# Optimization experiments

Hardware: AMD Instinct MI355X
Metric: run time of the kernel (lower is better)

Reference implementation:

```python
import jax, jax.numpy as jnp
import numpy as np

SEQ, D, H, P, FINAL = 2048, 1024, 16, 64, 1024


def setup_inputs() -> dict:
    key = jax.random.key(0)
    k_x, k_q, k_k, k_v, k_w = jax.random.split(key, 5)
    return {
        "x": jax.random.normal(k_x, (SEQ, D), dtype=jnp.float32),
        "Qw": jax.random.uniform(k_q, (H, D, P), dtype=jnp.float32),
        "Kw": jax.random.uniform(k_k, (H, D, P), dtype=jnp.float32),
        "Vw": jax.random.uniform(k_v, (H, D, P), dtype=jnp.float32),
        "W_fin": jax.random.normal(k_w, (H * P, FINAL), dtype=jnp.float32) * (1.0 / np.sqrt(H * P)),
        "b_fin": jnp.zeros((FINAL,), dtype=jnp.float32),
    }


def reference(x, Qw, Kw, Vw, W_fin, b_fin):
    # x: [S, D]; Qw/Kw/Vw: [H, D, P]
    Q = jnp.einsum("sd,hdp->hsp", x, Qw)  # [H, S, P]
    K = jnp.einsum("sd,hdp->hsp", x, Kw)
    V = jnp.einsum("sd,hdp->hsp", x, Vw)
    p_dim = K.shape[-1]
    # sigmoid attention: no row-wise normalization, scale by P (not sqrt(P))
    score = jax.nn.sigmoid(jnp.einsum("hsp,htp->hst", Q, K) / p_dim)  # [H, S, S]
    attn = jnp.einsum("hst,htp->hsp", score, V)  # [H, S, P]
    # faithful raw reshape (torch .reshape(seq, -1) on contiguous [H, S, P])
    concat = attn.reshape(x.shape[0], -1)  # [S, H*P]
    return concat @ W_fin + b_fin  # [S, FINAL]
```

## Files before the change

### kernel.cpp

```cpp
#include <hip/hip_runtime.h>
#include <hip/hip_bf16.h>

#define SEQL 2048
#define DMODEL 1024
#define NH 16
#define HEADP 64
#define FINALD 1024

using bf16x8 = __attribute__((ext_vector_type(8))) short;
using f32x4  = __attribute__((ext_vector_type(4))) float;
using s16x4  = __attribute__((ext_vector_type(4))) short;

#define WAITV(N) asm volatile("s_waitcnt vmcnt(" #N ")" ::: "memory")

__device__ __forceinline__ f32x4 mfma16(bf16x8 a, bf16x8 b, f32x4 c) {
  return __builtin_amdgcn_mfma_f32_16x16x32_bf16(a, b, c, 0, 0, 0);
}

__device__ __forceinline__ unsigned short f2bf(float f) {
  return __builtin_bit_cast(unsigned short, __float2bfloat16(f));
}

__device__ __forceinline__ void gload16(const void* g, void* l) {
  __builtin_amdgcn_global_load_lds(
      (const __attribute__((address_space(1))) void*)g,
      (__attribute__((address_space(3))) void*)l, 16, 0, 0);
}

__global__ __launch_bounds__(256) void k_prep(
    const float* __restrict__ Qw, const float* __restrict__ Kw,
    const float* __restrict__ Vw, const float* __restrict__ Wf,
    const float* __restrict__ x,
    unsigned short* __restrict__ Wt, unsigned short* __restrict__ WfT,
    unsigned short* __restrict__ xb) {
  __shared__ float tile[64][65];
  int z = blockIdx.z;
  int t = threadIdx.x;
  if (z == 4) {
    long i0 = ((long)blockIdx.y * 16 + blockIdx.x) * 2048 + t;
#pragma unroll
    for (int k = 0; k < 8; ++k) {
      long i = i0 + k * 256;
      float4 v = reinterpret_cast<const float4*>(x)[i];
      ushort4 o;
      o.x = f2bf(v.x); o.y = f2bf(v.y); o.z = f2bf(v.z); o.w = f2bf(v.w);
      reinterpret_cast<ushort4*>(xb)[i] = o;
    }
    return;
  }
  const float* src; unsigned short* dst;
  int C, tr = blockIdx.x * 64, tc;
  if (z < 3) {
    const float* s3 = (z == 0) ? Qw : (z == 1) ? Kw : Vw;
    src = s3 + (long)blockIdx.y * 65536;
    dst = Wt + (long)z * 1048576 + (long)blockIdx.y * 65536;
    C = 64; tc = 0;
  } else {
    src = Wf; dst = WfT; C = 1024; tc = blockIdx.y * 64;
  }
  const int R = 1024;
  int r0 = t >> 4, c4 = (t & 15) * 4;
#pragma unroll
  for (int i = 0; i < 4; ++i) {
    int r = i * 16 + r0;
    float4 v = *reinterpret_cast<const float4*>(src + (long)(tr + r) * C + tc + c4);
    tile[r][c4 + 0] = v.x; tile[r][c4 + 1] = v.y;
    tile[r][c4 + 2] = v.z; tile[r][c4 + 3] = v.w;
  }
  __syncthreads();
  int r4 = (t & 15) * 4, cc0 = t >> 4;
#pragma unroll
  for (int i = 0; i < 4; ++i) {
    int c = i * 16 + cc0;
    ushort4 o;
    o.x = f2bf(tile[r4 + 0][c]); o.y = f2bf(tile[r4 + 1][c]);
    o.z = f2bf(tile[r4 + 2][c]); o.w = f2bf(tile[r4 + 3][c]);
    *reinterpret_cast<ushort4*>(dst + (long)(tc + c) * R + tr + r4) = o;
  }
}

template <int EPI>
__global__ __launch_bounds__(256) void k_gemm(
    const unsigned short* __restrict__ A,
    const unsigned short* __restrict__ Bt,
    int K,
    unsigned short* __restrict__ Qb,
    unsigned short* __restrict__ Kb,
    unsigned short* __restrict__ Vtb,
    const float* __restrict__ bias,
    float* __restrict__ outf) {
  __shared__ char lds[49152];
  int flat = blockIdx.y * 16 + blockIdx.x;
  int cpx = (gridDim.x * gridDim.y) >> 3;
  flat = (flat & 7) * cpx + (flat >> 3);
  int m0 = (flat & 15) << 7, n0 = (flat >> 4) * 64;
  int t = threadIdx.x;
  int l = t & 63, w = t >> 6;
  int r = l & 15, g = l >> 4;
  int wr = w >> 1, wc = w & 1;

  const unsigned short* Arow = A + (long)m0 * K;
  const unsigned short* Brow = Bt + (long)n0 * K;
  int rr = l >> 2;
  int c8s = (((l & 3) ^ ((l >> 3) & 3)) * 8);

  auto stage = [&](int buf, int k0) {
    char* base = lds + buf * 24576;
#pragma unroll
    for (int kk = 0; kk < 2; ++kk) {
      char* dA = base + kk * 8192 + w * 2048;
      char* dB = base + 16384 + kk * 4096 + w * 1024;
      int kc = k0 + kk * 32 + c8s;
      gload16(Arow + (long)(w * 32 + rr) * K + kc, dA);
      gload16(Arow + (long)(w * 32 + 16 + rr) * K + kc, dA + 1024);
      gload16(Brow + (long)(w * 16 + rr) * K + kc, dB);
    }
  };

  int xk = (r >> 1) & 3;
  f32x4 acc[4][2] = {};
  int cur = 0, NK = K / 64;
  stage(0, 0);
  for (int kt = 0; kt < NK; ++kt) {
    __builtin_amdgcn_s_barrier();
    if (kt + 1 < NK) {
      stage(cur ^ 1, (kt + 1) * 64);
      WAITV(6);
    } else {
      WAITV(0);
    }
    __builtin_amdgcn_s_barrier();
    __builtin_amdgcn_sched_barrier(0);
    const char* base = lds + cur * 24576;
#pragma unroll
    for (int kk = 0; kk < 2; ++kk) {
      const char* As = base + kk * 8192;
      const char* Bs = base + 16384 + kk * 4096;
      bf16x8 af[4], bb[2];
#pragma unroll
      for (int i = 0; i < 4; ++i)
        af[i] = *reinterpret_cast<const bf16x8*>(As + (wr * 64 + i * 16 + r) * 64 + ((g ^ xk) * 16));
#pragma unroll
      for (int i = 0; i < 2; ++i)
        bb[i] = *reinterpret_cast<const bf16x8*>(Bs + (wc * 32 + i * 16 + r) * 64 + ((g ^ xk) * 16));
#pragma unroll
      for (int mi = 0; mi < 4; ++mi)
#pragma unroll
        for (int ni = 0; ni < 2; ++ni)
          acc[mi][ni] = mfma16(af[mi], bb[ni], acc[mi][ni]);
    }
    cur ^= 1;
  }

  if constexpr (EPI == 0) {
    int which = n0 >> 10;
    int hb = (n0 & 1023) >> 6;
    if (which < 2) {
      unsigned short* dst = (which == 0 ? Qb : Kb) + (long)hb * SEQL * HEADP;
#pragma unroll
      for (int mi = 0; mi < 4; ++mi) {
        int s0 = m0 + wr * 64 + mi * 16 + g * 4;
#pragma unroll
        for (int ni = 0; ni < 2; ++ni) {
          int p = wc * 32 + ni * 16 + r;
#pragma unroll
          for (int v = 0; v < 4; ++v)
            dst[(long)(s0 + v) * HEADP + p] = f2bf(acc[mi][ni][v]);
        }
      }
    } else {
      unsigned short* dst = Vtb + (long)hb * HEADP * SEQL;
#pragma unroll
      for (int mi = 0; mi < 4; ++mi) {
        int s0 = m0 + wr * 64 + mi * 16 + g * 4;
#pragma unroll
        for (int ni = 0; ni < 2; ++ni) {
          int p = wc * 32 + ni * 16 + r;
          ushort4 pk;
          pk.x = f2bf(acc[mi][ni][0]); pk.y = f2bf(acc[mi][ni][1]);
          pk.z = f2bf(acc[mi][ni][2]); pk.w = f2bf(acc[mi][ni][3]);
          *reinterpret_cast<ushort4*>(dst + (long)p * SEQL + s0) = pk;
        }
      }
    }
  } else {
#pragma unroll
    for (int ni = 0; ni < 2; ++ni) {
      int c = n0 + wc * 32 + ni * 16 + r;
      float bv = bias[c];
#pragma unroll
      for (int mi = 0; mi < 4; ++mi) {
        int s0 = m0 + wr * 64 + mi * 16 + g * 4;
#pragma unroll
        for (int v = 0; v < 4; ++v)
          outf[(long)(s0 + v) * FINALD + c] = acc[mi][ni][v] + bv;
      }
    }
  }
}

__global__ __launch_bounds__(256) void k_attn(
    const unsigned short* __restrict__ Qb,
    const unsigned short* __restrict__ Kb,
    const unsigned short* __restrict__ Vtb,
    unsigned short* __restrict__ Ab) {
  __shared__ char lds[40960];
  int b = blockIdx.x;
  int xcd = b & 7, j = b >> 3;
  int h = (xcd << 1) | (j & 1);
  int sblk = j >> 1;
  int lane = threadIdx.x & 63, wave = threadIdx.x >> 6;
  int r = lane & 15, g = lane >> 4;
  int q0 = sblk * 64 + wave * 16;
  const unsigned short* Qh = Qb + ((long)h * SEQL + q0) * HEADP;
  const unsigned short* Kh = Kb + (long)h * SEQL * HEADP;
  const unsigned short* Vh = Vtb + (long)h * HEADP * SEQL;

  bf16x8 qf0 = *reinterpret_cast<const bf16x8*>(Qh + (long)r * HEADP + g * 8);
  bf16x8 qf1 = *reinterpret_cast<const bf16x8*>(Qh + (long)r * HEADP + 32 + g * 8);

  f32x4 z4 = {0.f, 0.f, 0.f, 0.f};
  f32x4 oacc[4] = {z4, z4, z4, z4};
  char* slab = lds + 32768 + wave * 2048;
  int swz = (r & 7) << 4;
  const float CLN = -0.02254211001389005f;

  int sub = lane >> 3, chunk = lane & 7;
  auto stage = [&](int buf, int t0) {
    char* kb = lds + buf * 16384 + wave * 2048;
    char* vb = kb + 8192;
#pragma unroll
    for (int jj = 0; jj < 2; ++jj) {
      int row = wave * 16 + jj * 8 + sub;
      int sw = (chunk ^ (row & 7)) * 8;
      gload16(Kh + (long)(t0 + row) * HEADP + sw, kb + jj * 1024);
      gload16(Vh + (long)row * SEQL + t0 + sw, vb + jj * 1024);
    }
  };

  int cur = 0;
  stage(0, 0);
  for (int t0 = 0; t0 < SEQL; t0 += 64) {
    __builtin_amdgcn_s_barrier();
    if (t0 + 64 < SEQL) {
      stage(cur ^ 1, t0 + 64);
      WAITV(4);
    } else {
      WAITV(0);
    }
    __builtin_amdgcn_s_barrier();
    __builtin_amdgcn_sched_barrier(0);

    const char* kb = lds + cur * 16384;
    const char* vb = kb + 8192;
    f32x4 s[4] = {z4, z4, z4, z4};
    __builtin_amdgcn_s_setprio(1);
#pragma unroll
    for (int tb = 0; tb < 4; ++tb) {
      const char* krow = kb + (tb * 16 + r) * 128;
      bf16x8 k0 = *reinterpret_cast<const bf16x8*>(krow + ((g ^ (r & 7)) * 16));
      bf16x8 k1 = *reinterpret_cast<const bf16x8*>(krow + (((4 + g) ^ (r & 7)) * 16));
      s[tb] = mfma16(k0, qf0, s[tb]);
      s[tb] = mfma16(k1, qf1, s[tb]);
    }
    __builtin_amdgcn_s_setprio(0);
#pragma unroll
    for (int tb = 0; tb < 4; ++tb) {
      s16x4 pk;
#pragma unroll
      for (int v = 0; v < 4; ++v) {
        float e = __builtin_amdgcn_exp2f(s[tb][v] * CLN);
        pk[v] = (short)f2bf(__builtin_amdgcn_rcpf(1.0f + e));
      }
      *reinterpret_cast<s16x4*>(slab + r * 128 + ((tb * 32 + g * 8) ^ swz)) = pk;
    }
    bf16x8 pa0 = *reinterpret_cast<const bf16x8*>(slab + r * 128 + ((g * 16) ^ swz));
    bf16x8 pa1 = *reinterpret_cast<const bf16x8*>(slab + r * 128 + ((64 + g * 16) ^ swz));
    __builtin_amdgcn_s_setprio(1);
#pragma unroll
    for (int nb = 0; nb < 4; ++nb) {
      const char* vrow = vb + (nb * 16 + r) * 128;
      bf16x8 v0 = *reinterpret_cast<const bf16x8*>(vrow + ((g ^ (r & 7)) * 16));
      bf16x8 v1 = *reinterpret_cast<const bf16x8*>(vrow + (((4 + g) ^ (r & 7)) * 16));
      oacc[nb] = mfma16(pa0, v0, oacc[nb]);
      oacc[nb] = mfma16(pa1, v1, oacc[nb]);
    }
    __builtin_amdgcn_s_setprio(0);
    cur ^= 1;
  }
  unsigned short* Oh = Ab + ((long)h * SEQL + q0) * HEADP;
#pragma unroll
  for (int nb = 0; nb < 4; ++nb)
#pragma unroll
    for (int v = 0; v < 4; ++v)
      Oh[(g * 4 + v) * HEADP + nb * 16 + r] = f2bf(oacc[nb][v]);
}

extern "C" void kernel_launch(void* const* d_in, const int* in_sizes, int n_in,
                              void* d_out, int out_size, void* d_ws, size_t ws_size,
                              hipStream_t stream) {
  const float* x  = (const float*)d_in[0];
  const float* Qw = (const float*)d_in[1];
  const float* Kw = (const float*)d_in[2];
  const float* Vw = (const float*)d_in[3];
  const float* Wf = (const float*)d_in[4];
  const float* bf = (const float*)d_in[5];
  float* out = (float*)d_out;

  unsigned short* ws  = (unsigned short*)d_ws;
  unsigned short* xb  = ws;
  unsigned short* Wt  = ws + 2097152;
  unsigned short* WfT = ws + 5242880;
  unsigned short* Qb  = ws + 6291456;
  unsigned short* Kb  = ws + 8388608;
  unsigned short* Vtb = ws + 10485760;
  unsigned short* Ab  = ws + 12582912;

  k_prep<<<dim3(16, 16, 5), 256, 0, stream>>>(Qw, Kw, Vw, Wf, x, Wt, WfT, xb);
  k_gemm<0><<<dim3(16, 48), 256, 0, stream>>>(xb, Wt, DMODEL, Qb, Kb, Vtb, nullptr, nullptr);
  k_attn<<<512, 256, 0, stream>>>(Qb, Kb, Vtb, Ab);
  k_gemm<1><<<dim3(16, 16), 256, 0, stream>>>(Ab, WfT, DMODEL, nullptr, nullptr, nullptr, bf, out);
}
```

Before: 77.72 us.

## Process 32 query rows per wave in attention to reuse K/V tiles

Each wave in the sigmoid-attention kernel now handles two 16-row query blocks, so a block covers 128 queries and the grid halves to 256 blocks. Every K and V fragment loaded from LDS feeds twice as many MFMAs, which halves K/V global and LDS traffic per query. In exchange, registers and LDS per block grow (the P slab doubles), and only 256 blocks run on a 256-CU part, so latency hiding may drop.

Result: slower. 79.90 us (+2.8%).

```diff
diff --git a/kernel.cpp b/kernel.cpp
--- a/kernel.cpp
+++ b/kernel.cpp
@@ -204,24 +204,28 @@
     const unsigned short* __restrict__ Kb,
     const unsigned short* __restrict__ Vtb,
     unsigned short* __restrict__ Ab) {
-  __shared__ char lds[40960];
+  __shared__ char lds[49152];
   int b = blockIdx.x;
   int xcd = b & 7, j = b >> 3;
   int h = (xcd << 1) | (j & 1);
   int sblk = j >> 1;
   int lane = threadIdx.x & 63, wave = threadIdx.x >> 6;
   int r = lane & 15, g = lane >> 4;
-  int q0 = sblk * 64 + wave * 16;
+  int q0 = sblk * 128 + wave * 32;
   const unsigned short* Qh = Qb + ((long)h * SEQL + q0) * HEADP;
   const unsigned short* Kh = Kb + (long)h * SEQL * HEADP;
   const unsigned short* Vh = Vtb + (long)h * HEADP * SEQL;
 
-  bf16x8 qf0 = *reinterpret_cast<const bf16x8*>(Qh + (long)r * HEADP + g * 8);
-  bf16x8 qf1 = *reinterpret_cast<const bf16x8*>(Qh + (long)r * HEADP + 32 + g * 8);
+  bf16x8 qf[2][2];
+#pragma unroll
+  for (int qb = 0; qb < 2; ++qb) {
+    qf[qb][0] = *reinterpret_cast<const bf16x8*>(Qh + (long)(qb * 16 + r) * HEADP + g * 8);
+    qf[qb][1] = *reinterpret_cast<const bf16x8*>(Qh + (long)(qb * 16 + r) * HEADP + 32 + g * 8);
+  }
 
   f32x4 z4 = {0.f, 0.f, 0.f, 0.f};
-  f32x4 oacc[4] = {z4, z4, z4, z4};
-  char* slab = lds + 32768 + wave * 2048;
+  f32x4 oacc[2][4] = {{z4, z4, z4, z4}, {z4, z4, z4, z4}};
+  char* slab = lds + 32768 + wave * 4096;
   int swz = (r & 7) << 4;
   const float CLN = -0.02254211001389005f;
 
@@ -253,47 +257,61 @@
 
     const char* kb = lds + cur * 16384;
     const char* vb = kb + 8192;
-    f32x4 s[4] = {z4, z4, z4, z4};
+    f32x4 s[2][4] = {{z4, z4, z4, z4}, {z4, z4, z4, z4}};
     __builtin_amdgcn_s_setprio(1);
 #pragma unroll
     for (int tb = 0; tb < 4; ++tb) {
       const char* krow = kb + (tb * 16 + r) * 128;
       bf16x8 k0 = *reinterpret_cast<const bf16x8*>(krow + ((g ^ (r & 7)) * 16));
       bf16x8 k1 = *reinterpret_cast<const bf16x8*>(krow + (((4 + g) ^ (r & 7)) * 16));
-      s[tb] = mfma16(k0, qf0, s[tb]);
-      s[tb] = mfma16(k1, qf1, s[tb]);
+#pragma unroll
+      for (int qb = 0; qb < 2; ++qb) {
+        s[qb][tb] = mfma16(k0, qf[qb][0], s[qb][tb]);
+        s[qb][tb] = mfma16(k1, qf[qb][1], s[qb][tb]);
+      }
     }
     __builtin_amdgcn_s_setprio(0);
 #pragma unroll
-    for (int tb = 0; tb < 4; ++tb) {
-      s16x4 pk;
-#pragma unroll
-      for (int v = 0; v < 4; ++v) {
-        float e = __builtin_amdgcn_exp2f(s[tb][v] * CLN);
-        pk[v] = (short)f2bf(__builtin_amdgcn_rcpf(1.0f + e));
-      }
-      *reinterpret_cast<s16x4*>(slab + r * 128 + ((tb * 32 + g * 8) ^ swz)) = pk;
-    }
-    bf16x8 pa0 = *reinterpret_cast<const bf16x8*>(slab + r * 128 + ((g * 16) ^ swz));
-    bf16x8 pa1 = *reinterpret_cast<const bf16x8*>(slab + r * 128 + ((64 + g * 16) ^ swz));
+    for (int qb = 0; qb < 2; ++qb)
+#pragma unroll
+      for (int tb = 0; tb < 4; ++tb) {
+        s16x4 pk;
+#pragma unroll
+        for (int v = 0; v < 4; ++v) {
+          float e = __builtin_amdgcn_exp2f(s[qb][tb][v] * CLN);
+          pk[v] = (short)f2bf(__builtin_amdgcn_rcpf(1.0f + e));
+        }
+        *reinterpret_cast<s16x4*>(slab + (qb * 16 + r) * 128 + ((tb * 32 + g * 8) ^ swz)) = pk;
+      }
+    bf16x8 pa[2][2];
+#pragma unroll
+    for (int qb = 0; qb < 2; ++qb) {
+      pa[qb][0] = *reinterpret_cast<const bf16x8*>(slab + (qb * 16 + r) * 128 + ((g * 16) ^ swz));
+      pa[qb][1] = *reinterpret_cast<const bf16x8*>(slab + (qb * 16 + r) * 128 + ((64 + g * 16) ^ swz));
+    }
     __builtin_amdgcn_s_setprio(1);
 #pragma unroll
     for (int nb = 0; nb < 4; ++nb) {
       const char* vrow = vb + (nb * 16 + r) * 128;
       bf16x8 v0 = *reinterpret_cast<const bf16x8*>(vrow + ((g ^ (r & 7)) * 16));
       bf16x8 v1 = *reinterpret_cast<const bf16x8*>(vrow + (((4 + g) ^ (r & 7)) * 16));
-      oacc[nb] = mfma16(pa0, v0, oacc[nb]);
-      oacc[nb] = mfma16(pa1, v1, oacc[nb]);
+#pragma unroll
+      for (int qb = 0; qb < 2; ++qb) {
+        oacc[qb][nb] = mfma16(pa[qb][0], v0, oacc[qb][nb]);
+        oacc[qb][nb] = mfma16(pa[qb][1], v1, oacc[qb][nb]);
+      }
     }
     __builtin_amdgcn_s_setprio(0);
     cur ^= 1;
   }
   unsigned short* Oh = Ab + ((long)h * SEQL + q0) * HEADP;
 #pragma unroll
-  for (int nb = 0; nb < 4; ++nb)
-#pragma unroll
-    for (int v = 0; v < 4; ++v)
-      Oh[(g * 4 + v) * HEADP + nb * 16 + r] = f2bf(oacc[nb][v]);
+  for (int qb = 0; qb < 2; ++qb)
+#pragma unroll
+    for (int nb = 0; nb < 4; ++nb)
+#pragma unroll
+      for (int v = 0; v < 4; ++v)
+        Oh[(long)(qb * 16 + g * 4 + v) * HEADP + nb * 16 + r] = f2bf(oacc[qb][nb][v]);
 }
 
 extern "C" void kernel_launch(void* const* d_in, const int* in_sizes, int n_in,
@@ -318,6 +336,6 @@
 
   k_prep<<<dim3(16, 16, 5), 256, 0, stream>>>(Qw, Kw, Vw, Wf, x, Wt, WfT, xb);
   k_gemm<0><<<dim3(16, 48), 256, 0, stream>>>(xb, Wt, DMODEL, Qb, Kb, Vtb, nullptr, nullptr);
-  k_attn<<<512, 256, 0, stream>>>(Qb, Kb, Vtb, Ab);
+  k_attn<<<256, 256, 0, stream>>>(Qb, Kb, Vtb, Ab);
   k_gemm<1><<<dim3(16, 16), 256, 0, stream>>>(Ab, WfT, DMODEL, nullptr, nullptr, nullptr, bf, out);
 }
```

## Split attention key range across two blocks and add a reduce kernel

Applied to the files above, without the earlier changes.

The attention kernel now splits the key/value sequence into two halves, launching twice as many blocks. Each block writes fp32 partial outputs into scratch buffers that reuse the output and workspace memory. A new reduce kernel sums the two partials and converts the result to bf16 for the final GEMM. The aim is more parallelism and occupancy in attention, at the cost of extra global memory traffic and one more kernel launch.

Result: slower. 80.89 us (+4.1%).

```diff
diff --git a/kernel.cpp b/kernel.cpp
--- a/kernel.cpp
+++ b/kernel.cpp
@@ -203,12 +203,13 @@
     const unsigned short* __restrict__ Qb,
     const unsigned short* __restrict__ Kb,
     const unsigned short* __restrict__ Vtb,
-    unsigned short* __restrict__ Ab) {
+    float* __restrict__ P0, float* __restrict__ P1) {
   __shared__ char lds[40960];
   int b = blockIdx.x;
   int xcd = b & 7, j = b >> 3;
   int h = (xcd << 1) | (j & 1);
-  int sblk = j >> 1;
+  int sblk = (j >> 1) & 31;
+  int tc = j >> 6;
   int lane = threadIdx.x & 63, wave = threadIdx.x >> 6;
   int r = lane & 15, g = lane >> 4;
   int q0 = sblk * 64 + wave * 16;
@@ -238,11 +239,12 @@
     }
   };
 
+  int tbeg = tc * (SEQL / 2), tend = tbeg + SEQL / 2;
   int cur = 0;
-  stage(0, 0);
-  for (int t0 = 0; t0 < SEQL; t0 += 64) {
+  stage(0, tbeg);
+  for (int t0 = tbeg; t0 < tend; t0 += 64) {
     __builtin_amdgcn_s_barrier();
-    if (t0 + 64 < SEQL) {
+    if (t0 + 64 < tend) {
       stage(cur ^ 1, t0 + 64);
       WAITV(4);
     } else {
@@ -288,12 +290,24 @@
     __builtin_amdgcn_s_setprio(0);
     cur ^= 1;
   }
-  unsigned short* Oh = Ab + ((long)h * SEQL + q0) * HEADP;
+  float* Po = (tc ? P1 : P0) + ((long)h * SEQL + q0) * HEADP;
 #pragma unroll
   for (int nb = 0; nb < 4; ++nb)
 #pragma unroll
     for (int v = 0; v < 4; ++v)
-      Oh[(g * 4 + v) * HEADP + nb * 16 + r] = f2bf(oacc[nb][v]);
+      Po[(g * 4 + v) * HEADP + nb * 16 + r] = oacc[nb][v];
+}
+
+__global__ void k_reduce(const float* __restrict__ P0, const float* __restrict__ P1,
+                         unsigned short* __restrict__ Ab, int n4) {
+  int i = blockIdx.x * blockDim.x + threadIdx.x;
+  if (i >= n4) return;
+  float4 a = reinterpret_cast<const float4*>(P0)[i];
+  float4 b = reinterpret_cast<const float4*>(P1)[i];
+  ushort4 o;
+  o.x = f2bf(a.x + b.x); o.y = f2bf(a.y + b.y);
+  o.z = f2bf(a.z + b.z); o.w = f2bf(a.w + b.w);
+  reinterpret_cast<ushort4*>(Ab)[i] = o;
 }
 
 extern "C" void kernel_launch(void* const* d_in, const int* in_sizes, int n_in,
@@ -315,9 +329,12 @@
   unsigned short* Kb  = ws + 8388608;
   unsigned short* Vtb = ws + 10485760;
   unsigned short* Ab  = ws + 12582912;
+  float* P0 = (float*)d_out;
+  float* P1 = (float*)d_ws;
 
   k_prep<<<dim3(16, 16, 5), 256, 0, stream>>>(Qw, Kw, Vw, Wf, x, Wt, WfT, xb);
   k_gemm<0><<<dim3(16, 48), 256, 0, stream>>>(xb, Wt, DMODEL, Qb, Kb, Vtb, nullptr, nullptr);
-  k_attn<<<512, 256, 0, stream>>>(Qb, Kb, Vtb, Ab);
+  k_attn<<<1024, 256, 0, stream>>>(Qb, Kb, Vtb, P0, P1);
+  k_reduce<<<2048, 256, 0, stream>>>(P0, P1, Ab, 524288);
   k_gemm<1><<<dim3(16, 16), 256, 0, stream>>>(Ab, WfT, DMODEL, nullptr, nullptr, nullptr, bf, out);
 }
```

## Fuse all four stages into one cooperative persistent kernel with grid syncs

Applied to the files above, without the earlier changes.

Replaces the four separate launches (prep, QKV GEMM, attention, output GEMM) with a single cooperative kernel of 512 blocks that runs each stage as a loop over work units, separated by grid-wide syncs. The goal is to remove per-launch overhead and the gaps between kernels. In exchange, blocks are capped at 2 per CU by launch bounds, the grid syncs add their own cost, and stages whose work does not divide evenly into 512 blocks (1280 prep units, 768 GEMM tiles, 256 final tiles) leave blocks idle. The old multi-kernel path remains as a fallback if the cooperative launch fails.

Result: slower. 290.3 us (+273.5%).

```diff
diff --git a/kernel.cpp b/kernel.cpp
--- a/kernel.cpp
+++ b/kernel.cpp
@@ -1,5 +1,8 @@
 #include <hip/hip_runtime.h>
 #include <hip/hip_bf16.h>
+#include <hip/hip_cooperative_groups.h>
+
+namespace cg = cooperative_groups;
 
 #define SEQL 2048
 #define DMODEL 1024
@@ -27,17 +30,15 @@
       (__attribute__((address_space(3))) void*)l, 16, 0, 0);
 }
 
-__global__ __launch_bounds__(256) void k_prep(
-    const float* __restrict__ Qw, const float* __restrict__ Kw,
-    const float* __restrict__ Vw, const float* __restrict__ Wf,
-    const float* __restrict__ x,
-    unsigned short* __restrict__ Wt, unsigned short* __restrict__ WfT,
-    unsigned short* __restrict__ xb) {
-  __shared__ float tile[64][65];
-  int z = blockIdx.z;
+__device__ __forceinline__ void prep_unit(
+    int u, const float* Qw, const float* Kw, const float* Vw,
+    const float* Wf, const float* x,
+    unsigned short* Wt, unsigned short* WfT, unsigned short* xb,
+    char* ldsbuf) {
   int t = threadIdx.x;
+  int z = u >> 8;
   if (z == 4) {
-    long i0 = ((long)blockIdx.y * 16 + blockIdx.x) * 2048 + t;
+    long i0 = (long)(u & 255) * 2048 + t;
 #pragma unroll
     for (int k = 0; k < 8; ++k) {
       long i = i0 + k * 256;
@@ -48,17 +49,20 @@
     }
     return;
   }
+  float (*tile)[65] = (float(*)[65])ldsbuf;
+  int ux = u & 15, uy = (u >> 4) & 15;
   const float* src; unsigned short* dst;
-  int C, tr = blockIdx.x * 64, tc;
+  int C, tr = ux * 64, tc;
   if (z < 3) {
     const float* s3 = (z == 0) ? Qw : (z == 1) ? Kw : Vw;
-    src = s3 + (long)blockIdx.y * 65536;
-    dst = Wt + (long)z * 1048576 + (long)blockIdx.y * 65536;
+    src = s3 + (long)uy * 65536;
+    dst = Wt + (long)z * 1048576 + (long)uy * 65536;
     C = 64; tc = 0;
   } else {
-    src = Wf; dst = WfT; C = 1024; tc = blockIdx.y * 64;
+    src = Wf; dst = WfT; C = 1024; tc = uy * 64;
   }
   const int R = 1024;
+  __syncthreads();
   int r0 = t >> 4, c4 = (t & 15) * 4;
 #pragma unroll
   for (int i = 0; i < 4; ++i) {
@@ -80,19 +84,13 @@
 }
 
 template <int EPI>
-__global__ __launch_bounds__(256) void k_gemm(
-    const unsigned short* __restrict__ A,
-    const unsigned short* __restrict__ Bt,
-    int K,
-    unsigned short* __restrict__ Qb,
-    unsigned short* __restrict__ Kb,
-    unsigned short* __restrict__ Vtb,
-    const float* __restrict__ bias,
-    float* __restrict__ outf) {
-  __shared__ char lds[49152];
-  int flat = blockIdx.y * 16 + blockIdx.x;
-  int cpx = (gridDim.x * gridDim.y) >> 3;
-  flat = (flat & 7) * cpx + (flat >> 3);
+__device__ __forceinline__ void gemm_tile(
+    char* lds, int u, int ntiles,
+    const unsigned short* A, const unsigned short* Bt, int K,
+    unsigned short* Qb, unsigned short* Kb, unsigned short* Vtb,
+    const float* bias, float* outf) {
+  int cpx = ntiles >> 3;
+  int flat = (u & 7) * cpx + (u >> 3);
   int m0 = (flat & 15) << 7, n0 = (flat >> 4) * 64;
   int t = threadIdx.x;
   int l = t & 63, w = t >> 6;
@@ -199,13 +197,10 @@
   }
 }
 
-__global__ __launch_bounds__(256) void k_attn(
-    const unsigned short* __restrict__ Qb,
-    const unsigned short* __restrict__ Kb,
-    const unsigned short* __restrict__ Vtb,
-    unsigned short* __restrict__ Ab) {
-  __shared__ char lds[40960];
-  int b = blockIdx.x;
+__device__ __forceinline__ void attn_block(
+    char* lds, int b,
+    const unsigned short* Qb, const unsigned short* Kb,
+    const unsigned short* Vtb, unsigned short* Ab) {
   int xcd = b & 7, j = b >> 3;
   int h = (xcd << 1) | (j & 1);
   int sblk = j >> 1;
@@ -294,6 +289,60 @@
 #pragma unroll
     for (int v = 0; v < 4; ++v)
       Oh[(g * 4 + v) * HEADP + nb * 16 + r] = f2bf(oacc[nb][v]);
+}
+
+__global__ __launch_bounds__(256, 2) void k_mega(
+    const float* __restrict__ x,  const float* __restrict__ Qw,
+    const float* __restrict__ Kw, const float* __restrict__ Vw,
+    const float* __restrict__ Wf, const float* __restrict__ bfin,
+    unsigned short* xb, unsigned short* Wt, unsigned short* WfT,
+    unsigned short* Qb, unsigned short* Kb, unsigned short* Vtb,
+    unsigned short* Ab, float* out) {
+  __shared__ char lds[49152];
+  cg::grid_group grid = cg::this_grid();
+  int bid = blockIdx.x;
+
+  for (int u = bid; u < 1280; u += 512)
+    prep_unit(u, Qw, Kw, Vw, Wf, x, Wt, WfT, xb, lds);
+  grid.sync();
+
+  for (int u = bid; u < 768; u += 512)
+    gemm_tile<0>(lds, u, 768, xb, Wt, DMODEL, Qb, Kb, Vtb, nullptr, nullptr);
+  grid.sync();
+
+  attn_block(lds, bid, Qb, Kb, Vtb, Ab);
+  grid.sync();
+
+  if (bid < 256)
+    gemm_tile<1>(lds, bid, 256, Ab, WfT, DMODEL, nullptr, nullptr, nullptr, bfin, out);
+}
+
+__global__ __launch_bounds__(256) void k_prep(
+    const float* __restrict__ Qw, const float* __restrict__ Kw,
+    const float* __restrict__ Vw, const float* __restrict__ Wf,
+    const float* __restrict__ x,
+    unsigned short* Wt, unsigned short* WfT, unsigned short* xb) {
+  __shared__ char lds[16640];
+  int u = blockIdx.z * 256 + blockIdx.y * 16 + blockIdx.x;
+  prep_unit(u, Qw, Kw, Vw, Wf, x, Wt, WfT, xb, lds);
+}
+
+template <int EPI>
+__global__ __launch_bounds__(256) void k_gemm(
+    const unsigned short* __restrict__ A, const unsigned short* __restrict__ Bt,
+    int K, int ntiles,
+    unsigned short* Qb, unsigned short* Kb, unsigned short* Vtb,
+    const float* bias, float* outf) {
+  __shared__ char lds[49152];
+  int u = blockIdx.y * 16 + blockIdx.x;
+  gemm_tile<EPI>(lds, u, ntiles, A, Bt, K, Qb, Kb, Vtb, bias, outf);
+}
+
+__global__ __launch_bounds__(256) void k_attn(
+    const unsigned short* __restrict__ Qb, const unsigned short* __restrict__ Kb,
+    const unsigned short* __restrict__ Vtb, unsigned short* Ab) {
+  __shared__ char lds[40960];
+  attn_block(lds, blockIdx.x, Qb, Kb, Vtb, Ab);
 }
 
 extern "C" void kernel_launch(void* const* d_in, const int* in_sizes, int n_in,
@@ -316,8 +365,16 @@
   unsigned short* Vtb = ws + 10485760;
   unsigned short* Ab  = ws + 12582912;
 
-  k_prep<<<dim3(16, 16, 5), 256, 0, stream>>>(Qw, Kw, Vw, Wf, x, Wt, WfT, xb);
-  k_gemm<0><<<dim3(16, 48), 256, 0, stream>>>(xb, Wt, DMODEL, Qb, Kb, Vtb, nullptr, nullptr);
-  k_attn<<<512, 256, 0, stream>>>(Qb, Kb, Vtb, Ab);
-  k_gemm<1><<<dim3(16, 16), 256, 0, stream>>>(Ab, WfT, DMODEL, nullptr, nullptr, nullptr, bf, out);
-}
+  void* args[] = {(void*)&x, (void*)&Qw, (void*)&Kw, (void*)&Vw, (void*)&Wf,
+                  (void*)&bf, (void*)&xb, (void*)&Wt, (void*)&WfT, (void*)&Qb,
+                  (void*)&Kb, (void*)&Vtb, (void*)&Ab, (void*)&out};
+  hipError_t err = hipLaunchCooperativeKernel(
+      (void*)k_mega, dim3(512), dim3(256), args, 0, stream);
+  if (err != hipSuccess) {
+    (void)hipGetLastError();
+    k_prep<<<dim3(16, 16, 5), 256, 0, stream>>>(Qw, Kw, Vw, Wf, x, Wt, WfT, xb);
+    k_gemm<0><<<dim3(16, 48), 256, 0, stream>>>(xb, Wt, DMODEL, 768, Qb, Kb, Vtb, nullptr, nullptr);
+    k_attn<<<512, 256, 0, stream>>>(Qb, Kb, Vtb, Ab);
+    k_gemm<1><<<dim3(16, 16), 256, 0, stream>>>(Ab, WfT, DMODEL, 256, nullptr, nullptr, nullptr, bf, out);
+  }
+}
```
